# Kernel optimization log

Hardware: AMD Instinct MI355X
Metric: run time of the kernel (lower is better)

## Reference

```python
import jax, jax.numpy as jnp
import numpy as np

N_NODES = 50000
N_EDGES = 600000
IN_CH = 128
OUT_CH = 128


def setup_inputs() -> dict:
    key = jax.random.key(0)
    k1, k2, k3, k4 = jax.random.split(key, 4)
    x = jax.random.normal(k1, (N_NODES, IN_CH), dtype=jnp.float32)
    edge_index = jax.random.randint(k2, (2, N_EDGES), 0, N_NODES, dtype=jnp.int64)
    W_msg = jax.random.normal(k3, (OUT_CH, IN_CH * 9), dtype=jnp.float32) * (1.0 / np.sqrt(IN_CH * 9))
    b_msg = jnp.zeros((OUT_CH,), dtype=jnp.float32)
    W_root = jax.random.normal(k4, (OUT_CH, IN_CH), dtype=jnp.float32) * (1.0 / np.sqrt(IN_CH))
    b_root = jnp.zeros((OUT_CH,), dtype=jnp.float32)
    return {"x": x, "edge_index": edge_index, "W_msg": W_msg, "b_msg": b_msg,
            "W_root": W_root, "b_root": b_root}


def reference(x, edge_index, W_msg, b_msg, W_root, b_root):
    n = x.shape[0]
    src = edge_index[0]
    dst = edge_index[1]

    # in-degree per destination node
    degree = jax.ops.segment_sum(jnp.ones_like(dst, dtype=x.dtype), dst, num_segments=n)  # [N]

    msgs = x[src]  # [E, C] gathered source features
    agg_sum = jax.ops.segment_sum(msgs, dst, num_segments=n)                 # [N, C]
    agg_mean = agg_sum / jnp.maximum(degree, 1.0)[:, None]                    # [N, C]
    agg_max = jax.ops.segment_max(msgs, dst, num_segments=n)                  # [N, C], -inf for empty
    agg_max = jnp.where(degree[:, None] > 0, agg_max, 0.0)

    degree_term = jnp.log1p(degree + 1.0)[:, None]                            # [N, 1]
    degree_reference = jnp.maximum(jnp.mean(jnp.log1p(degree + 1.0)), 1.0)    # scalar

    amp = degree_term / degree_reference                                       # [N, 1]
    att = degree_reference / jnp.maximum(degree_term, 1e-06)                   # [N, 1]

    feats = []
    for agg in (agg_sum, agg_mean, agg_max):
        feats.append(agg)            # identity
        feats.append(agg * amp)      # amplification
        feats.append(agg * att)      # attenuation
    stacked = jnp.concatenate(feats, axis=-1)                                  # [N, 9C]

    return stacked @ W_msg.T + b_msg + x @ W_root.T + b_root
```

## Files before the change

### kernel.cpp

```cpp
#include <hip/hip_runtime.h>
#include <cmath>

#define IN_CH 128
#define OUT_CH 128
#define KDIM 512
#define NGEMM 384
#define GBM 256
#define GBN 192
#define SLOT_B 40960
#define SLOT_US 20480
#define PIPE_LDS_BYTES (3 * SLOT_B)

typedef __attribute__((ext_vector_type(8))) short bfrag;
typedef __attribute__((ext_vector_type(4))) float f32x4;

__device__ __forceinline__ unsigned short f2bf(float f) {
    unsigned int u = __float_as_uint(f);
    return (unsigned short)((u + 0x7FFFu + ((u >> 16) & 1u)) >> 16);
}
__device__ __forceinline__ float bf2f(unsigned short h) {
    return __uint_as_float(((unsigned int)h) << 16);
}
__device__ __forceinline__ float4 unpack4(uint2 u) {
    float4 r;
    r.x = __uint_as_float(u.x << 16);
    r.y = __uint_as_float(u.x & 0xFFFF0000u);
    r.z = __uint_as_float(u.y << 16);
    r.w = __uint_as_float(u.y & 0xFFFF0000u);
    return r;
}

__device__ __forceinline__ void gl2lds16(const void* g, void* l) {
    __builtin_amdgcn_global_load_lds(
        (const __attribute__((address_space(1))) unsigned int*)g,
        (__attribute__((address_space(3))) unsigned int*)l, 16, 0, 0);
}


__global__ void degree_kernel(const int* __restrict__ ei, int* __restrict__ degree, int E) {
    int e = blockIdx.x * blockDim.x + threadIdx.x;
    if (e < E) atomicAdd(&degree[ei[E + e]], 1);
}

__global__ __launch_bounds__(256) void scan1_kernel(const int* __restrict__ degree,
                                                    int* __restrict__ part,
                                                    float* __restrict__ partlog, int n) {
    int i = blockIdx.x * 256 + threadIdx.x;
    int d = (i < n) ? degree[i] : 0;
    float lg = (i < n) ? logf((float)d + 2.0f) : 0.f;
    #pragma unroll
    for (int off = 32; off; off >>= 1) {
        d += __shfl_down(d, off);
        lg += __shfl_down(lg, off);
    }
    __shared__ int sd[4];
    __shared__ float sl[4];
    int wv = threadIdx.x >> 6;
    if ((threadIdx.x & 63) == 0) { sd[wv] = d; sl[wv] = lg; }
    __syncthreads();
    if (threadIdx.x == 0) {
        part[blockIdx.x] = (sd[0] + sd[1]) + (sd[2] + sd[3]);
        partlog[blockIdx.x] = (sl[0] + sl[1]) + (sl[2] + sl[3]);
    }
}

__global__ __launch_bounds__(256) void scan2_kernel(int* __restrict__ part,
                                                    const float* __restrict__ partlog,
                                                    float* __restrict__ logsum, int B) {
    int tid = threadIdx.x, lane = tid & 63, wv = tid >> 6;
    __shared__ int wsum[4];
    __shared__ float wl[4];
    __shared__ int carry_s;
    if (tid == 0) carry_s = 0;
    float lg = 0.f;
    __syncthreads();
    for (int base0 = 0; base0 < B; base0 += 256) {
        int idx = base0 + tid;
        int v = (idx < B) ? part[idx] : 0;
        if (idx < B) lg += partlog[idx];
        int s = v;
        #pragma unroll
        for (int off = 1; off < 64; off <<= 1) {
            int t = __shfl_up(s, off);
            if (lane >= off) s += t;
        }
        if (lane == 63) wsum[wv] = s;
        __syncthreads();
        int wbase = carry_s;
        for (int w2 = 0; w2 < wv; ++w2) wbase += wsum[w2];
        if (idx < B) part[idx] = wbase + s - v;
        __syncthreads();
        if (tid == 0) carry_s += (wsum[0] + wsum[1]) + (wsum[2] + wsum[3]);
        __syncthreads();
    }
    #pragma unroll
    for (int off = 32; off; off >>= 1) lg += __shfl_down(lg, off);
    if (lane == 0) wl[wv] = lg;
    __syncthreads();
    if (tid == 0) logsum[0] = (wl[0] + wl[1]) + (wl[2] + wl[3]);
}

__global__ __launch_bounds__(256) void scan3_kernel(const int* __restrict__ degree,
                                                    const int* __restrict__ part,
                                                    int* __restrict__ offsets, int n, int E) {
    int i = blockIdx.x * 256 + threadIdx.x;
    int d = (i < n) ? degree[i] : 0;
    int lane = threadIdx.x & 63, wv = threadIdx.x >> 6;
    int s = d;
    #pragma unroll
    for (int off = 1; off < 64; off <<= 1) {
        int t = __shfl_up(s, off);
        if (lane >= off) s += t;
    }
    __shared__ int wsum[4];
    if (lane == 63) wsum[wv] = s;
    __syncthreads();
    int base = part[blockIdx.x];
    for (int w2 = 0; w2 < wv; ++w2) base += wsum[w2];
    if (i < n) offsets[i] = base + s - d;
    if (i == n - 1) offsets[n] = E;
}

__global__ void fill_kernel(const int* __restrict__ ei, int* __restrict__ offsets,
                            int* __restrict__ csr_src, int E) {
    int e = blockIdx.x * blockDim.x + threadIdx.x;
    if (e < E) {
        int src = ei[e];
        int dst = ei[E + e];
        int pos = atomicAdd(&offsets[dst], 1);
        csr_src[pos] = src;
    }
}


__global__ void xcast_kernel(const float* __restrict__ x, unsigned short* __restrict__ xb,
                             int total4) {
    int i = blockIdx.x * 256 + threadIdx.x;
    if (i >= total4) return;
    float4 v = ((const float4*)x)[i];
    uint2 p;
    p.x = (unsigned)f2bf(v.x) | ((unsigned)f2bf(v.y) << 16);
    p.y = (unsigned)f2bf(v.z) | ((unsigned)f2bf(v.w) << 16);
    ((uint2*)xb)[i] = p;
}


__global__ __launch_bounds__(256) void agg_kernel(const unsigned short* __restrict__ xb,
                                                  const int* __restrict__ csr_src,
                                                  const int* __restrict__ offsets,
                                                  const int* __restrict__ degree,
                                                  const float* __restrict__ logsum,
                                                  unsigned short* __restrict__ Zhi,
                                                  float* __restrict__ ampv,
                                                  float* __restrict__ attv,
                                                  int N, int Mpad) {
    int node = (blockIdx.x * 256 + threadIdx.x) >> 6;
    int lane = threadIdx.x & 63;
    if (node >= Mpad) return;
    int h = lane >> 5;
    int c4 = lane & 31;
    long zbase = (long)node * KDIM + c4 * 4;
    if (node >= N) {
        if (h == 0) {
            uint2 z = make_uint2(0u, 0u);
            #pragma unroll
            for (int sec = 0; sec < 4; ++sec) *(uint2*)&Zhi[zbase + sec * 128] = z;
        }
        return;
    }
    int deg = degree[node];
    int end = offsets[node];
    int beg = end - deg;
    const float NEG = -3.402823466e38f;
    float4 s[4], m[4];
    #pragma unroll
    for (int u = 0; u < 4; ++u) {
        s[u] = make_float4(0.f, 0.f, 0.f, 0.f);
        m[u] = make_float4(NEG, NEG, NEG, NEG);
    }
    int i = beg;
    for (; i + 8 <= end; i += 8) {
        int idx[4];
        #pragma unroll
        for (int u = 0; u < 4; ++u) idx[u] = csr_src[i + u * 2 + h];
        uint2 raw[4];
        #pragma unroll
        for (int u = 0; u < 4; ++u) raw[u] = *(const uint2*)&xb[(long)idx[u] * IN_CH + c4 * 4];
        #pragma unroll
        for (int u = 0; u < 4; ++u) {
            float4 v = unpack4(raw[u]);
            s[u].x += v.x; s[u].y += v.y; s[u].z += v.z; s[u].w += v.w;
            m[u].x = fmaxf(m[u].x, v.x); m[u].y = fmaxf(m[u].y, v.y);
            m[u].z = fmaxf(m[u].z, v.z); m[u].w = fmaxf(m[u].w, v.w);
        }
    }
    for (; i < end; i += 2) {
        int e = i + h;
        if (e < end) {
            float4 v = unpack4(*(const uint2*)&xb[(long)csr_src[e] * IN_CH + c4 * 4]);
            s[0].x += v.x; s[0].y += v.y; s[0].z += v.z; s[0].w += v.w;
            m[0].x = fmaxf(m[0].x, v.x); m[0].y = fmaxf(m[0].y, v.y);
            m[0].z = fmaxf(m[0].z, v.z); m[0].w = fmaxf(m[0].w, v.w);
        }
    }
    float4 sum, mx;
    sum.x = (s[0].x + s[1].x) + (s[2].x + s[3].x);
    sum.y = (s[0].y + s[1].y) + (s[2].y + s[3].y);
    sum.z = (s[0].z + s[1].z) + (s[2].z + s[3].z);
    sum.w = (s[0].w + s[1].w) + (s[2].w + s[3].w);
    mx.x = fmaxf(fmaxf(m[0].x, m[1].x), fmaxf(m[2].x, m[3].x));
    mx.y = fmaxf(fmaxf(m[0].y, m[1].y), fmaxf(m[2].y, m[3].y));
    mx.z = fmaxf(fmaxf(m[0].z, m[1].z), fmaxf(m[2].z, m[3].z));
    mx.w = fmaxf(fmaxf(m[0].w, m[1].w), fmaxf(m[2].w, m[3].w));
    sum.x += __shfl_xor(sum.x, 32); sum.y += __shfl_xor(sum.y, 32);
    sum.z += __shfl_xor(sum.z, 32); sum.w += __shfl_xor(sum.w, 32);
    mx.x = fmaxf(mx.x, __shfl_xor(mx.x, 32)); mx.y = fmaxf(mx.y, __shfl_xor(mx.y, 32));
    mx.z = fmaxf(mx.z, __shfl_xor(mx.z, 32)); mx.w = fmaxf(mx.w, __shfl_xor(mx.w, 32));

    float inv = 1.0f / fmaxf((float)deg, 1.0f);
    float4 mean = make_float4(sum.x * inv, sum.y * inv, sum.z * inv, sum.w * inv);
    if (deg == 0) mx = make_float4(0.f, 0.f, 0.f, 0.f);
    float4 xv = unpack4(*(const uint2*)&xb[(long)node * IN_CH + c4 * 4]);

    if (h == 0) {
        float4 secs[4] = { xv, sum, mean, mx };
        #pragma unroll
        for (int sec = 0; sec < 4; ++sec) {
            float4 v = secs[sec];
            uint2 hi;
            hi.x = (unsigned)f2bf(v.x) | ((unsigned)f2bf(v.y) << 16);
            hi.y = (unsigned)f2bf(v.z) | ((unsigned)f2bf(v.w) << 16);
            *(uint2*)&Zhi[zbase + sec * 128] = hi;
        }
    }
    if (lane == 0) {
        float ref = fmaxf(logsum[0] / (float)N, 1.0f);
        float dt = log1pf((float)deg + 1.0f);
        ampv[node] = dt / ref;
        attv[node] = ref / fmaxf(dt, 1e-6f);
    }
}


__global__ void wbuild_kernel(const float* __restrict__ Wmsg, const float* __restrict__ Wroot,
                              unsigned short* __restrict__ Whi, unsigned short* __restrict__ Wlo) {
    int idx = blockIdx.x * 256 + threadIdx.x;
    if (idx >= NGEMM * KDIM) return;
    int jp = idx >> 9;
    int k = idx & 511;
    int cg = jp / 96;
    int rem = jp - cg * 96;
    int s16 = rem >> 4;
    int r16 = rem & 15;
    int wn2 = s16 / 3;
    int sec = s16 - wn2 * 3;
    int ocol = cg * 32 + wn2 * 16 + r16;
    float v;
    if (k < 128) {
        v = (sec == 0) ? Wroot[ocol * 128 + k] : 0.f;
    } else {
        int a = (k - 128) >> 7;
        int c = (k - 128) & 127;
        v = Wmsg[ocol * 1152 + (a * 3 + sec) * 128 + c];
    }
    unsigned short h = f2bf(v);
    Whi[idx] = h;
    Wlo[idx] = f2bf(v - bf2f(h));
}


__global__ __launch_bounds__(1024, 4) void gemm_pipe(const unsigned short* __restrict__ Zhi,
                                                     const unsigned short* __restrict__ Whi,
                                                     const unsigned short* __restrict__ Wlo,
                                                     const float* __restrict__ ampv,
                                                     const float* __restrict__ attv,
                                                     const float* __restrict__ bmsg,
                                                     const float* __restrict__ broot,
                                                     float* __restrict__ out, int M) {
    extern __shared__ char smem[];
    unsigned short* lds = (unsigned short*)smem;
    const int tid = threadIdx.x;
    const int w = tid >> 6;
    const int lane = tid & 63;
    const int r16 = lane & 15, q = lane >> 4;
    const int wm = w >> 2, wn = w & 3;
    const int row0 = blockIdx.x * GBM;
    const int cg2 = blockIdx.y;

    const unsigned short* sAh = Zhi + (long)(row0 + w * 16 + r16) * KDIM + q * 8;
    const unsigned short* sB2 = (w < 12)
        ? Whi + (long)(cg2 * GBN + w * 16 + r16) * KDIM + q * 8
        : Wlo + (long)(cg2 * GBN + (w - 12) * 16 + r16) * KDIM + q * 8;
    const unsigned short* sB3 = Wlo + (long)(cg2 * GBN + (4 + w) * 16 + r16) * KDIM + q * 8;
    const int d0 = tid * 16, d2 = (1024 + tid) * 16, d3 = (2048 + tid) * 16;

    gl2lds16(sAh, smem + d0); gl2lds16(sB2, smem + d2); if (w < 8) gl2lds16(sB3, smem + d3);
    sAh += 32; sB2 += 32; sB3 += 32;
    gl2lds16(sAh, smem + SLOT_B + d0); gl2lds16(sB2, smem + SLOT_B + d2);
    if (w < 8) gl2lds16(sB3, smem + SLOT_B + d3);
    sAh += 32; sB2 += 32; sB3 += 32;

    if (w < 8) __builtin_amdgcn_s_waitcnt(0x0F73);
    else       __builtin_amdgcn_s_waitcnt(0x0F72);
    __builtin_amdgcn_s_barrier();
    __builtin_amdgcn_sched_barrier(0);

    f32x4 acc[4][3] = {};
    const int jtb = (wn >> 1) * 6 + (wn & 1) * 3;

    #pragma unroll 1
    for (int it = 0; it < 16; ++it) {
        const int s = it % 3;
        if (it + 2 < 16) {
            char* b = smem + ((it + 2) % 3) * SLOT_B;
            gl2lds16(sAh, b + d0); gl2lds16(sB2, b + d2); if (w < 8) gl2lds16(sB3, b + d3);
            sAh += 32; sB2 += 32; sB3 += 32;
        }
        const unsigned short* L = lds + s * SLOT_US;

        bfrag bh[3], bl[3];
        #pragma unroll
        for (int nt = 0; nt < 3; ++nt) {
            int chb = (jtb + nt) * 512 + lane * 8;
            bh[nt] = *(const bfrag*)&L[8192 + chb];
            bl[nt] = *(const bfrag*)&L[14336 + chb];
        }
        #pragma unroll
        for (int mt = 0; mt < 4; ++mt) {
            bfrag ah = *(const bfrag*)&L[((wm * 4 + mt) * 64 + lane) * 8];
            #pragma unroll
            for (int nt = 0; nt < 3; ++nt) {
                acc[mt][nt] = __builtin_amdgcn_mfma_f32_16x16x32_bf16(ah, bh[nt], acc[mt][nt], 0, 0, 0);
                acc[mt][nt] = __builtin_amdgcn_mfma_f32_16x16x32_bf16(ah, bl[nt], acc[mt][nt], 0, 0, 0);
            }
        }

        if (it < 14) {
            if (w < 8) __builtin_amdgcn_s_waitcnt(0x0F73);
            else       __builtin_amdgcn_s_waitcnt(0x0F72);
        } else if (it == 14) {
            __builtin_amdgcn_s_waitcnt(0x0F70);
        }
        if (it < 15) {
            __builtin_amdgcn_s_barrier();
            __builtin_amdgcn_sched_barrier(0);
        }
    }

    const int col = (cg2 * 2 + (wn >> 1)) * 32 + (wn & 1) * 16 + r16;
    const float bias = bmsg[col] + broot[col];
    #pragma unroll
    for (int mt = 0; mt < 4; ++mt) {
        #pragma unroll
        for (int r = 0; r < 4; ++r) {
            int row = row0 + wm * 64 + mt * 16 + q * 4 + r;
            if (row < M) {
                float v = acc[mt][0][r]
                        + ampv[row] * acc[mt][1][r]
                        + attv[row] * acc[mt][2][r] + bias;
                out[(long)row * OUT_CH + col] = v;
            }
        }
    }
}


__global__ __launch_bounds__(1024, 4) void gemm_sb(const unsigned short* __restrict__ Zhi,
                                                   const unsigned short* __restrict__ Whi,
                                                   const unsigned short* __restrict__ Wlo,
                                                   const float* __restrict__ ampv,
                                                   const float* __restrict__ attv,
                                                   const float* __restrict__ bmsg,
                                                   const float* __restrict__ broot,
                                                   float* __restrict__ out, int M) {
    __shared__ unsigned short lds[SLOT_US];
    const int tid = threadIdx.x;
    const int w = tid >> 6;
    const int lane = tid & 63;
    const int r16 = lane & 15, q = lane >> 4;
    const int wm = w >> 2, wn = w & 3;
    const int row0 = blockIdx.x * GBM;
    const int cg2 = blockIdx.y;

    const unsigned short* sAh = Zhi + (long)(row0 + w * 16 + r16) * KDIM + q * 8;
    const unsigned short* sB2 = (w < 12)
        ? Whi + (long)(cg2 * GBN + w * 16 + r16) * KDIM + q * 8
        : Wlo + (long)(cg2 * GBN + (w - 12) * 16 + r16) * KDIM + q * 8;
    const unsigned short* sB3 = Wlo + (long)(cg2 * GBN + (4 + w) * 16 + r16) * KDIM + q * 8;
    char* ldsb = (char*)lds;
    const int d0 = tid * 16, d2 = (1024 + tid) * 16, d3 = (2048 + tid) * 16;

    f32x4 acc[4][3] = {};
    const int jtb = (wn >> 1) * 6 + (wn & 1) * 3;

    #pragma unroll 1
    for (int it = 0; it < 16; ++it) {
        if (it) __syncthreads();
        gl2lds16(sAh, ldsb + d0); gl2lds16(sB2, ldsb + d2); if (w < 8) gl2lds16(sB3, ldsb + d3);
        sAh += 32; sB2 += 32; sB3 += 32;
        __syncthreads();

        bfrag bh[3], bl[3];
        #pragma unroll
        for (int nt = 0; nt < 3; ++nt) {
            int chb = (jtb + nt) * 512 + lane * 8;
            bh[nt] = *(const bfrag*)&lds[8192 + chb];
            bl[nt] = *(const bfrag*)&lds[14336 + chb];
        }
        #pragma unroll
        for (int mt = 0; mt < 4; ++mt) {
            bfrag ah = *(const bfrag*)&lds[((wm * 4 + mt) * 64 + lane) * 8];
            #pragma unroll
            for (int nt = 0; nt < 3; ++nt) {
                acc[mt][nt] = __builtin_amdgcn_mfma_f32_16x16x32_bf16(ah, bh[nt], acc[mt][nt], 0, 0, 0);
                acc[mt][nt] = __builtin_amdgcn_mfma_f32_16x16x32_bf16(ah, bl[nt], acc[mt][nt], 0, 0, 0);
            }
        }
    }

    const int col = (cg2 * 2 + (wn >> 1)) * 32 + (wn & 1) * 16 + r16;
    const float bias = bmsg[col] + broot[col];
    #pragma unroll
    for (int mt = 0; mt < 4; ++mt) {
        #pragma unroll
        for (int r = 0; r < 4; ++r) {
            int row = row0 + wm * 64 + mt * 16 + q * 4 + r;
            if (row < M) {
                float v = acc[mt][0][r]
                        + ampv[row] * acc[mt][1][r]
                        + attv[row] * acc[mt][2][r] + bias;
                out[(long)row * OUT_CH + col] = v;
            }
        }
    }
}


extern "C" void kernel_launch(void* const* d_in, const int* in_sizes, int n_in,
                              void* d_out, int out_size, void* d_ws, size_t ws_size,
                              hipStream_t stream) {
    const float* x     = (const float*)d_in[0];
    const int*   ei    = (const int*)d_in[1];
    const float* Wmsg  = (const float*)d_in[2];
    const float* bmsg  = (const float*)d_in[3];
    const float* Wroot = (const float*)d_in[4];
    const float* broot = (const float*)d_in[5];
    float* out = (float*)d_out;

    int N = in_sizes[0] / IN_CH;
    int E = in_sizes[1] / 2;
    int Mb = (N + GBM - 1) / GBM;
    int Mpad = Mb * GBM;
    int Sb = (N + 255) / 256;

    char* ws = (char*)d_ws;
    size_t off = 0;
    auto alloc = [&](size_t bytes) -> void* {
        void* p = ws + off;
        off = (off + bytes + 255) & ~(size_t)255;
        return p;
    };
    int* degree  = (int*)alloc((size_t)N * 4);
    int* offsets = (int*)alloc((size_t)(N + 1) * 4);
    float* logsum = (float*)alloc(4);
    int* part    = (int*)alloc((size_t)Sb * 4);
    float* partlog = (float*)alloc((size_t)Sb * 4);
    int* csr_src = (int*)alloc((size_t)E * 4);
    unsigned short* Whi = (unsigned short*)alloc((size_t)NGEMM * KDIM * 2);
    unsigned short* Wlo = (unsigned short*)alloc((size_t)NGEMM * KDIM * 2);
    unsigned short* Zhi = (unsigned short*)alloc((size_t)Mpad * KDIM * 2);
    unsigned short* xb  = (unsigned short*)alloc((size_t)Mpad * IN_CH * 2);
    float* ampv = (float*)alloc((size_t)N * 4);
    float* attv = (float*)alloc((size_t)N * 4);

    hipMemsetAsync(degree, 0, (size_t)N * 4, stream);

    degree_kernel<<<(E + 255) / 256, 256, 0, stream>>>(ei, degree, E);
    xcast_kernel<<<(N * IN_CH / 4 + 255) / 256, 256, 0, stream>>>(x, xb, N * IN_CH / 4);
    scan1_kernel<<<Sb, 256, 0, stream>>>(degree, part, partlog, N);
    scan2_kernel<<<1, 256, 0, stream>>>(part, partlog, logsum, Sb);
    scan3_kernel<<<Sb, 256, 0, stream>>>(degree, part, offsets, N, E);
    fill_kernel<<<(E + 255) / 256, 256, 0, stream>>>(ei, offsets, csr_src, E);
    agg_kernel<<<(Mpad * 64 + 255) / 256, 256, 0, stream>>>(xb, csr_src, offsets, degree, logsum,
                                                            Zhi, ampv, attv, N, Mpad);
    wbuild_kernel<<<(NGEMM * KDIM + 255) / 256, 256, 0, stream>>>(Wmsg, Wroot, Whi, Wlo);

    bool pipe = false;
    int dev = 0;
    if (hipGetDevice(&dev) == hipSuccess) {
        int optin = 0;
        if (hipDeviceGetAttribute(&optin, hipDeviceAttributeSharedMemPerBlockOptin, dev) == hipSuccess
            && optin >= (int)PIPE_LDS_BYTES) {
            pipe = (hipFuncSetAttribute((const void*)gemm_pipe,
                                        hipFuncAttributeMaxDynamicSharedMemorySize,
                                        PIPE_LDS_BYTES) == hipSuccess);
        }
    }
    dim3 ggrid(Mb, 2);
    if (pipe) {
        gemm_pipe<<<ggrid, 1024, PIPE_LDS_BYTES, stream>>>(Zhi, Whi, Wlo, ampv, attv,
                                                           bmsg, broot, out, N);
    } else {
        gemm_sb<<<ggrid, 1024, 0, stream>>>(Zhi, Whi, Wlo, ampv, attv,
                                            bmsg, broot, out, N);
    }
}
```

Before: 247.5 us.

## Shrink GEMM tile to 128 rows with 512 threads and double buffering

Replaces the 1024-thread, 256-row, triple-buffered pipelined GEMM with a 512-thread, 128-row variant that uses two LDS slots and reassigns the B-tile load mapping so each wave loads three 16-row chunks. Halving the M tile doubles the block count, which is meant to improve CU occupancy and load balance across the device. The LDS footprint drops from 120KB to 64KB, so more blocks may fit per CU. In exchange, prefetch depth falls from two stages to one, so global-to-LDS latency is less hidden, and each B tile is reloaded by twice as many blocks.

```diff
diff --git a/kernel.cpp b/kernel.cpp
--- a/kernel.cpp
+++ b/kernel.cpp
@@ -6,10 +6,13 @@
 #define KDIM 512
 #define NGEMM 384
 #define GBM 256
+#define GBM2 128
 #define GBN 192
 #define SLOT_B 40960
 #define SLOT_US 20480
-#define PIPE_LDS_BYTES (3 * SLOT_B)
+#define SLOT2_B 32768
+#define SLOT2_US 16384
+#define PIPE2_LDS_BYTES (2 * SLOT2_B)
 
 typedef __attribute__((ext_vector_type(8))) short bfrag;
 typedef __attribute__((ext_vector_type(4))) float f32x4;
@@ -269,7 +272,7 @@
 }
 
 
-__global__ __launch_bounds__(1024, 4) void gemm_pipe(const unsigned short* __restrict__ Zhi,
+__global__ __launch_bounds__(512, 4) void gemm_pipe2(const unsigned short* __restrict__ Zhi,
                                                      const unsigned short* __restrict__ Whi,
                                                      const unsigned short* __restrict__ Wlo,
                                                      const float* __restrict__ ampv,
@@ -284,24 +287,34 @@
     const int lane = tid & 63;
     const int r16 = lane & 15, q = lane >> 4;
     const int wm = w >> 2, wn = w & 3;
-    const int row0 = blockIdx.x * GBM;
+    const int row0 = blockIdx.x * GBM2;
     const int cg2 = blockIdx.y;
 
-    const unsigned short* sAh = Zhi + (long)(row0 + w * 16 + r16) * KDIM + q * 8;
-    const unsigned short* sB2 = (w < 12)
-        ? Whi + (long)(cg2 * GBN + w * 16 + r16) * KDIM + q * 8
-        : Wlo + (long)(cg2 * GBN + (w - 12) * 16 + r16) * KDIM + q * 8;
-    const unsigned short* sB3 = Wlo + (long)(cg2 * GBN + (4 + w) * 16 + r16) * KDIM + q * 8;
-    const int d0 = tid * 16, d2 = (1024 + tid) * 16, d3 = (2048 + tid) * 16;
-
-    gl2lds16(sAh, smem + d0); gl2lds16(sB2, smem + d2); if (w < 8) gl2lds16(sB3, smem + d3);
-    sAh += 32; sB2 += 32; sB3 += 32;
-    gl2lds16(sAh, smem + SLOT_B + d0); gl2lds16(sB2, smem + SLOT_B + d2);
-    if (w < 8) gl2lds16(sB3, smem + SLOT_B + d3);
-    sAh += 32; sB2 += 32; sB3 += 32;
-
-    if (w < 8) __builtin_amdgcn_s_waitcnt(0x0F73);
-    else       __builtin_amdgcn_s_waitcnt(0x0F72);
+    const unsigned short* sA = Zhi + (long)(row0 + w * 16 + r16) * KDIM + q * 8;
+    const unsigned short* sB0;
+    const unsigned short* sB1;
+    const unsigned short* sB2;
+    {
+        int b0 = w * 3;
+        const unsigned short* p[3];
+        #pragma unroll
+        for (int j = 0; j < 3; ++j) {
+            int b = b0 + j;
+            const unsigned short* Wb = (b < 12) ? Whi : Wlo;
+            int rrow = ((b < 12) ? b : (b - 12)) * 16;
+            p[j] = Wb + (long)(cg2 * GBN + rrow + r16) * KDIM + q * 8;
+        }
+        sB0 = p[0]; sB1 = p[1]; sB2 = p[2];
+    }
+    const int dA = tid * 16;
+    const int dB0 = 8192 + (w * 3 + 0) * 1024 + lane * 16;
+    const int dB1 = 8192 + (w * 3 + 1) * 1024 + lane * 16;
+    const int dB2 = 8192 + (w * 3 + 2) * 1024 + lane * 16;
+
+    gl2lds16(sA, smem + dA); gl2lds16(sB0, smem + dB0);
+    gl2lds16(sB1, smem + dB1); gl2lds16(sB2, smem + dB2);
+    sA += 32; sB0 += 32; sB1 += 32; sB2 += 32;
+    __builtin_amdgcn_s_waitcnt(0x0F70);
     __builtin_amdgcn_s_barrier();
     __builtin_amdgcn_sched_barrier(0);
 
@@ -310,20 +323,21 @@
 
     #pragma unroll 1
     for (int it = 0; it < 16; ++it) {
-        const int s = it % 3;
-        if (it + 2 < 16) {
-            char* b = smem + ((it + 2) % 3) * SLOT_B;
-            gl2lds16(sAh, b + d0); gl2lds16(sB2, b + d2); if (w < 8) gl2lds16(sB3, b + d3);
-            sAh += 32; sB2 += 32; sB3 += 32;
-        }
-        const unsigned short* L = lds + s * SLOT_US;
+        const int s = it & 1;
+        if (it + 1 < 16) {
+            char* b = smem + (s ^ 1) * SLOT2_B;
+            gl2lds16(sA, b + dA); gl2lds16(sB0, b + dB0);
+            gl2lds16(sB1, b + dB1); gl2lds16(sB2, b + dB2);
+            sA += 32; sB0 += 32; sB1 += 32; sB2 += 32;
+        }
+        const unsigned short* L = lds + s * SLOT2_US;
 
         bfrag bh[3], bl[3];
         #pragma unroll
         for (int nt = 0; nt < 3; ++nt) {
             int chb = (jtb + nt) * 512 + lane * 8;
-            bh[nt] = *(const bfrag*)&L[8192 + chb];
-            bl[nt] = *(const bfrag*)&L[14336 + chb];
+            bh[nt] = *(const bfrag*)&L[4096 + chb];
+            bl[nt] = *(const bfrag*)&L[10240 + chb];
         }
         #pragma unroll
         for (int mt = 0; mt < 4; ++mt) {
@@ -335,12 +349,7 @@
             }
         }
 
-        if (it < 14) {
-            if (w < 8) __builtin_amdgcn_s_waitcnt(0x0F73);
-            else       __builtin_amdgcn_s_waitcnt(0x0F72);
-        } else if (it == 14) {
-            __builtin_amdgcn_s_waitcnt(0x0F70);
-        }
+        if (it + 1 < 16) __builtin_amdgcn_s_waitcnt(0x0F70);
         if (it < 15) {
             __builtin_amdgcn_s_barrier();
             __builtin_amdgcn_sched_barrier(0);
@@ -451,6 +460,7 @@
     int E = in_sizes[1] / 2;
     int Mb = (N + GBM - 1) / GBM;
     int Mpad = Mb * GBM;
+    int Mb2 = (N + GBM2 - 1) / GBM2;
     int Sb = (N + 255) / 256;
 
     char* ws = (char*)d_ws;
@@ -490,17 +500,18 @@
     if (hipGetDevice(&dev) == hipSuccess) {
         int optin = 0;
         if (hipDeviceGetAttribute(&optin, hipDeviceAttributeSharedMemPerBlockOptin, dev) == hipSuccess
-            && optin >= (int)PIPE_LDS_BYTES) {
-            pipe = (hipFuncSetAttribute((const void*)gemm_pipe,
+            && optin >= (int)PIPE2_LDS_BYTES) {
+            pipe = (hipFuncSetAttribute((const void*)gemm_pipe2,
                                         hipFuncAttributeMaxDynamicSharedMemorySize,
-                                        PIPE_LDS_BYTES) == hipSuccess);
-        }
-    }
-    dim3 ggrid(Mb, 2);
+                                        PIPE2_LDS_BYTES) == hipSuccess);
+        }
+    }
     if (pipe) {
-        gemm_pipe<<<ggrid, 1024, PIPE_LDS_BYTES, stream>>>(Zhi, Whi, Wlo, ampv, attv,
-                                                           bmsg, broot, out, N);
+        dim3 ggrid(Mb2, 2);
+        gemm_pipe2<<<ggrid, 512, PIPE2_LDS_BYTES, stream>>>(Zhi, Whi, Wlo, ampv, attv,
+                                                            bmsg, broot, out, N);
     } else {
+        dim3 ggrid(Mb, 2);
         gemm_sb<<<ggrid, 1024, 0, stream>>>(Zhi, Whi, Wlo, ampv, attv,
                                             bmsg, broot, out, N);
     }
```

New measurement: 267.9 us. 1.08x slower.

## Rewrite pipelined GEMM with 32x32x16 MFMA and 512-thread blocks

Applied to the files above, without the earlier changes.

Replaces the 1024-thread pipelined GEMM, which used 16x16x32 bf16 MFMAs, with a 512-thread variant built on 32x32x16 MFMAs. Each wave now computes a 64x32 output tile with larger accumulators. The LDS fragment layout and the global-to-LDS copy assignment are redone so that hi and lo weight fragments sit p*6144 apart. The goal is fewer LDS fragment reads per MFMA and higher MFMA efficiency, at the cost of more accumulator registers per wave and fewer waves per block.

```diff
diff --git a/kernel.cpp b/kernel.cpp
--- a/kernel.cpp
+++ b/kernel.cpp
@@ -13,6 +13,7 @@
 
 typedef __attribute__((ext_vector_type(8))) short bfrag;
 typedef __attribute__((ext_vector_type(4))) float f32x4;
+typedef __attribute__((ext_vector_type(16))) float f32x16;
 
 __device__ __forceinline__ unsigned short f2bf(float f) {
     unsigned int u = __float_as_uint(f);
@@ -269,95 +270,104 @@
 }
 
 
-__global__ __launch_bounds__(1024, 4) void gemm_pipe(const unsigned short* __restrict__ Zhi,
-                                                     const unsigned short* __restrict__ Whi,
-                                                     const unsigned short* __restrict__ Wlo,
-                                                     const float* __restrict__ ampv,
-                                                     const float* __restrict__ attv,
-                                                     const float* __restrict__ bmsg,
-                                                     const float* __restrict__ broot,
-                                                     float* __restrict__ out, int M) {
+__global__ __launch_bounds__(512, 2) void gemm_pipe32(const unsigned short* __restrict__ Zhi,
+                                                      const unsigned short* __restrict__ Whi,
+                                                      const unsigned short* __restrict__ Wlo,
+                                                      const float* __restrict__ ampv,
+                                                      const float* __restrict__ attv,
+                                                      const float* __restrict__ bmsg,
+                                                      const float* __restrict__ broot,
+                                                      float* __restrict__ out, int M) {
     extern __shared__ char smem[];
     unsigned short* lds = (unsigned short*)smem;
     const int tid = threadIdx.x;
     const int w = tid >> 6;
     const int lane = tid & 63;
-    const int r16 = lane & 15, q = lane >> 4;
-    const int wm = w >> 2, wn = w & 3;
+    const int r16s = lane & 15, qs = lane >> 4;
+    const int wm = w >> 1, wn = w & 1;
     const int row0 = blockIdx.x * GBM;
     const int cg2 = blockIdx.y;
 
-    const unsigned short* sAh = Zhi + (long)(row0 + w * 16 + r16) * KDIM + q * 8;
-    const unsigned short* sB2 = (w < 12)
-        ? Whi + (long)(cg2 * GBN + w * 16 + r16) * KDIM + q * 8
-        : Wlo + (long)(cg2 * GBN + (w - 12) * 16 + r16) * KDIM + q * 8;
-    const unsigned short* sB3 = Wlo + (long)(cg2 * GBN + (4 + w) * 16 + r16) * KDIM + q * 8;
-    const int d0 = tid * 16, d2 = (1024 + tid) * 16, d3 = (2048 + tid) * 16;
-
-    gl2lds16(sAh, smem + d0); gl2lds16(sB2, smem + d2); if (w < 8) gl2lds16(sB3, smem + d3);
-    sAh += 32; sB2 += 32; sB3 += 32;
-    gl2lds16(sAh, smem + SLOT_B + d0); gl2lds16(sB2, smem + SLOT_B + d2);
-    if (w < 8) gl2lds16(sB3, smem + SLOT_B + d3);
-    sAh += 32; sB2 += 32; sB3 += 32;
-
-    if (w < 8) __builtin_amdgcn_s_waitcnt(0x0F73);
-    else       __builtin_amdgcn_s_waitcnt(0x0F72);
+    const unsigned short* sA0 = Zhi + (long)(row0 + (2 * w) * 16 + r16s) * KDIM + qs * 8;
+    const unsigned short* sA1 = sA0 + 16 * KDIM;
+    const unsigned short* Bb = (w < 4) ? Whi : Wlo;
+    const int c0 = (w < 4) ? 3 * w : 3 * (w - 4);
+    const unsigned short* sB0 = Bb + (long)(cg2 * GBN + c0 * 16 + r16s) * KDIM + qs * 8;
+    const unsigned short* sB1 = sB0 + 16 * KDIM;
+    const unsigned short* sB2 = sB0 + 32 * KDIM;
+    const int dA0 = (2 * w) * 1024 + lane * 16, dA1 = dA0 + 1024;
+    const int dB0 = 16384 + (3 * w) * 1024 + lane * 16;
+    const int dB1 = dB0 + 1024, dB2 = dB0 + 2048;
+
+    gl2lds16(sA0, smem + dA0); gl2lds16(sA1, smem + dA1);
+    gl2lds16(sB0, smem + dB0); gl2lds16(sB1, smem + dB1); gl2lds16(sB2, smem + dB2);
+    sA0 += 32; sA1 += 32; sB0 += 32; sB1 += 32; sB2 += 32;
+    gl2lds16(sA0, smem + SLOT_B + dA0); gl2lds16(sA1, smem + SLOT_B + dA1);
+    gl2lds16(sB0, smem + SLOT_B + dB0); gl2lds16(sB1, smem + SLOT_B + dB1);
+    gl2lds16(sB2, smem + SLOT_B + dB2);
+    sA0 += 32; sA1 += 32; sB0 += 32; sB1 += 32; sB2 += 32;
+
+    __builtin_amdgcn_s_waitcnt(0x0F75);
     __builtin_amdgcn_s_barrier();
     __builtin_amdgcn_sched_barrier(0);
 
-    f32x4 acc[4][3] = {};
-    const int jtb = (wn >> 1) * 6 + (wn & 1) * 3;
+    const int wn2r = (lane >> 4) & 1, khr = lane >> 5, r16r = lane & 15;
+    const int aBase = wm * 2048 + wn2r * 512 + khr * 128 + r16r * 8;
+    const int bBase = 8192 + wn * 3072 + wn2r * 1536 + khr * 128 + r16r * 8;
+
+    f32x16 acc[2][3] = {};
 
     #pragma unroll 1
     for (int it = 0; it < 16; ++it) {
         const int s = it % 3;
         if (it + 2 < 16) {
             char* b = smem + ((it + 2) % 3) * SLOT_B;
-            gl2lds16(sAh, b + d0); gl2lds16(sB2, b + d2); if (w < 8) gl2lds16(sB3, b + d3);
-            sAh += 32; sB2 += 32; sB3 += 32;
+            gl2lds16(sA0, b + dA0); gl2lds16(sA1, b + dA1);
+            gl2lds16(sB0, b + dB0); gl2lds16(sB1, b + dB1); gl2lds16(sB2, b + dB2);
+            sA0 += 32; sA1 += 32; sB0 += 32; sB1 += 32; sB2 += 32;
         }
         const unsigned short* L = lds + s * SLOT_US;
 
-        bfrag bh[3], bl[3];
-        #pragma unroll
-        for (int nt = 0; nt < 3; ++nt) {
-            int chb = (jtb + nt) * 512 + lane * 8;
-            bh[nt] = *(const bfrag*)&L[8192 + chb];
-            bl[nt] = *(const bfrag*)&L[14336 + chb];
-        }
-        #pragma unroll
-        for (int mt = 0; mt < 4; ++mt) {
-            bfrag ah = *(const bfrag*)&L[((wm * 4 + mt) * 64 + lane) * 8];
+        bfrag a[2][2];
+        #pragma unroll
+        for (int mt = 0; mt < 2; ++mt)
             #pragma unroll
-            for (int nt = 0; nt < 3; ++nt) {
-                acc[mt][nt] = __builtin_amdgcn_mfma_f32_16x16x32_bf16(ah, bh[nt], acc[mt][nt], 0, 0, 0);
-                acc[mt][nt] = __builtin_amdgcn_mfma_f32_16x16x32_bf16(ah, bl[nt], acc[mt][nt], 0, 0, 0);
+            for (int kh = 0; kh < 2; ++kh)
+                a[mt][kh] = *(const bfrag*)&L[aBase + mt * 1024 + kh * 256];
+
+        #pragma unroll
+        for (int kh = 0; kh < 2; ++kh) {
+            #pragma unroll
+            for (int p = 0; p < 2; ++p) {
+                #pragma unroll
+                for (int sec = 0; sec < 3; ++sec) {
+                    bfrag bf = *(const bfrag*)&L[bBase + sec * 512 + kh * 256 + p * 6144];
+                    acc[0][sec] = __builtin_amdgcn_mfma_f32_32x32x16_bf16(a[0][kh], bf, acc[0][sec], 0, 0, 0);
+                    acc[1][sec] = __builtin_amdgcn_mfma_f32_32x32x16_bf16(a[1][kh], bf, acc[1][sec], 0, 0, 0);
+                }
             }
         }
 
-        if (it < 14) {
-            if (w < 8) __builtin_amdgcn_s_waitcnt(0x0F73);
-            else       __builtin_amdgcn_s_waitcnt(0x0F72);
-        } else if (it == 14) {
-            __builtin_amdgcn_s_waitcnt(0x0F70);
-        }
+        if (it < 14)      __builtin_amdgcn_s_waitcnt(0x0F75);
+        else if (it == 14) __builtin_amdgcn_s_waitcnt(0x0F70);
         if (it < 15) {
             __builtin_amdgcn_s_barrier();
             __builtin_amdgcn_sched_barrier(0);
         }
     }
 
-    const int col = (cg2 * 2 + (wn >> 1)) * 32 + (wn & 1) * 16 + r16;
+    const int col = (cg2 * 2 + wn) * 32 + (lane & 31);
     const float bias = bmsg[col] + broot[col];
+    const int rb = row0 + wm * 64 + 4 * (lane >> 5);
     #pragma unroll
-    for (int mt = 0; mt < 4; ++mt) {
-        #pragma unroll
-        for (int r = 0; r < 4; ++r) {
-            int row = row0 + wm * 64 + mt * 16 + q * 4 + r;
+    for (int mt = 0; mt < 2; ++mt) {
+        #pragma unroll
+        for (int reg = 0; reg < 16; ++reg) {
+            int row = rb + mt * 32 + (reg & 3) + 8 * (reg >> 2);
             if (row < M) {
-                float v = acc[mt][0][r]
-                        + ampv[row] * acc[mt][1][r]
-                        + attv[row] * acc[mt][2][r] + bias;
+                float v = acc[mt][0][reg]
+                        + ampv[row] * acc[mt][1][reg]
+                        + attv[row] * acc[mt][2][reg] + bias;
                 out[(long)row * OUT_CH + col] = v;
             }
         }
@@ -491,15 +501,15 @@
         int optin = 0;
         if (hipDeviceGetAttribute(&optin, hipDeviceAttributeSharedMemPerBlockOptin, dev) == hipSuccess
             && optin >= (int)PIPE_LDS_BYTES) {
-            pipe = (hipFuncSetAttribute((const void*)gemm_pipe,
+            pipe = (hipFuncSetAttribute((const void*)gemm_pipe32,
                                         hipFuncAttributeMaxDynamicSharedMemorySize,
                                         PIPE_LDS_BYTES) == hipSuccess);
         }
     }
     dim3 ggrid(Mb, 2);
     if (pipe) {
-        gemm_pipe<<<ggrid, 1024, PIPE_LDS_BYTES, stream>>>(Zhi, Whi, Wlo, ampv, attv,
-                                                           bmsg, broot, out, N);
+        gemm_pipe32<<<ggrid, 512, PIPE_LDS_BYTES, stream>>>(Zhi, Whi, Wlo, ampv, attv,
+                                                            bmsg, broot, out, N);
     } else {
         gemm_sb<<<ggrid, 1024, 0, stream>>>(Zhi, Whi, Wlo, ampv, attv,
                                             bmsg, broot, out, N);
```

New measurement: 258.1 us. 4.3% more time.

## Fuse prep kernels, drop serial scan pass, and trim early GEMM k-steps

Applied to the files above, without the earlier changes.

Merges the degree count and the x-to-bf16 cast into one prep kernel. Removes the single-block scan2 kernel: each scan3 block now sums the preceding block partials itself, and the log-degree total is accumulated with a float atomic in scan1. The GEMM main loop is split so the first four k-steps issue MFMAs for only one N sub-tile, apparently relying on zero blocks in the packed weight layout to skip work. This cuts launches and the serial scan, but the float atomic makes logsum order nondeterministic, and the GEMM skip is only correct if those weight blocks really are zero.

```diff
diff --git a/kernel.cpp b/kernel.cpp
--- a/kernel.cpp
+++ b/kernel.cpp
@@ -37,14 +37,27 @@
 }
 
 
-__global__ void degree_kernel(const int* __restrict__ ei, int* __restrict__ degree, int E) {
-    int e = blockIdx.x * blockDim.x + threadIdx.x;
-    if (e < E) atomicAdd(&degree[ei[E + e]], 1);
+__global__ __launch_bounds__(256) void prep_kernel(const int* __restrict__ ei,
+                                                   int* __restrict__ degree,
+                                                   float* __restrict__ logsum,
+                                                   const float* __restrict__ x,
+                                                   unsigned short* __restrict__ xb,
+                                                   int E, int total4) {
+    int i = blockIdx.x * 256 + threadIdx.x;
+    if (i == 0) logsum[0] = 0.f;
+    if (i < E) atomicAdd(&degree[ei[E + i]], 1);
+    if (i < total4) {
+        float4 v = ((const float4*)x)[i];
+        uint2 p;
+        p.x = (unsigned)f2bf(v.x) | ((unsigned)f2bf(v.y) << 16);
+        p.y = (unsigned)f2bf(v.z) | ((unsigned)f2bf(v.w) << 16);
+        ((uint2*)xb)[i] = p;
+    }
 }
 
 __global__ __launch_bounds__(256) void scan1_kernel(const int* __restrict__ degree,
                                                     int* __restrict__ part,
-                                                    float* __restrict__ partlog, int n) {
+                                                    float* __restrict__ logsum, int n) {
     int i = blockIdx.x * 256 + threadIdx.x;
     int d = (i < n) ? degree[i] : 0;
     float lg = (i < n) ? logf((float)d + 2.0f) : 0.f;
@@ -60,52 +73,28 @@
     __syncthreads();
     if (threadIdx.x == 0) {
         part[blockIdx.x] = (sd[0] + sd[1]) + (sd[2] + sd[3]);
-        partlog[blockIdx.x] = (sl[0] + sl[1]) + (sl[2] + sl[3]);
-    }
-}
-
-__global__ __launch_bounds__(256) void scan2_kernel(int* __restrict__ part,
-                                                    const float* __restrict__ partlog,
-                                                    float* __restrict__ logsum, int B) {
-    int tid = threadIdx.x, lane = tid & 63, wv = tid >> 6;
-    __shared__ int wsum[4];
-    __shared__ float wl[4];
-    __shared__ int carry_s;
-    if (tid == 0) carry_s = 0;
-    float lg = 0.f;
-    __syncthreads();
-    for (int base0 = 0; base0 < B; base0 += 256) {
-        int idx = base0 + tid;
-        int v = (idx < B) ? part[idx] : 0;
-        if (idx < B) lg += partlog[idx];
-        int s = v;
-        #pragma unroll
-        for (int off = 1; off < 64; off <<= 1) {
-            int t = __shfl_up(s, off);
-            if (lane >= off) s += t;
-        }
-        if (lane == 63) wsum[wv] = s;
-        __syncthreads();
-        int wbase = carry_s;
-        for (int w2 = 0; w2 < wv; ++w2) wbase += wsum[w2];
-        if (idx < B) part[idx] = wbase + s - v;
-        __syncthreads();
-        if (tid == 0) carry_s += (wsum[0] + wsum[1]) + (wsum[2] + wsum[3]);
-        __syncthreads();
-    }
-    #pragma unroll
-    for (int off = 32; off; off >>= 1) lg += __shfl_down(lg, off);
-    if (lane == 0) wl[wv] = lg;
-    __syncthreads();
-    if (tid == 0) logsum[0] = (wl[0] + wl[1]) + (wl[2] + wl[3]);
+        atomicAdd(&logsum[0], (sl[0] + sl[1]) + (sl[2] + sl[3]));
+    }
 }
 
 __global__ __launch_bounds__(256) void scan3_kernel(const int* __restrict__ degree,
                                                     const int* __restrict__ part,
-                                                    int* __restrict__ offsets, int n, int E) {
-    int i = blockIdx.x * 256 + threadIdx.x;
+                                                    int* __restrict__ offsets,
+                                                    int n, int E, int Sb) {
+    int tid = threadIdx.x;
+    int i = blockIdx.x * 256 + tid;
+    int b = blockIdx.x;
+    int acc0 = 0;
+    for (int j = tid; j < b; j += 256) acc0 += part[j];
+    #pragma unroll
+    for (int off = 32; off; off >>= 1) acc0 += __shfl_down(acc0, off);
+    __shared__ int bsum[4];
+    int lane = tid & 63, wv = tid >> 6;
+    if (lane == 0) bsum[wv] = acc0;
+    __syncthreads();
+    int base = (bsum[0] + bsum[1]) + (bsum[2] + bsum[3]);
+
     int d = (i < n) ? degree[i] : 0;
-    int lane = threadIdx.x & 63, wv = threadIdx.x >> 6;
     int s = d;
     #pragma unroll
     for (int off = 1; off < 64; off <<= 1) {
@@ -115,7 +104,6 @@
     __shared__ int wsum[4];
     if (lane == 63) wsum[wv] = s;
     __syncthreads();
-    int base = part[blockIdx.x];
     for (int w2 = 0; w2 < wv; ++w2) base += wsum[w2];
     if (i < n) offsets[i] = base + s - d;
     if (i == n - 1) offsets[n] = E;
@@ -130,18 +118,6 @@
         int pos = atomicAdd(&offsets[dst], 1);
         csr_src[pos] = src;
     }
-}
-
-
-__global__ void xcast_kernel(const float* __restrict__ x, unsigned short* __restrict__ xb,
-                             int total4) {
-    int i = blockIdx.x * 256 + threadIdx.x;
-    if (i >= total4) return;
-    float4 v = ((const float4*)x)[i];
-    uint2 p;
-    p.x = (unsigned)f2bf(v.x) | ((unsigned)f2bf(v.y) << 16);
-    p.y = (unsigned)f2bf(v.z) | ((unsigned)f2bf(v.w) << 16);
-    ((uint2*)xb)[i] = p;
 }
 
 
@@ -309,7 +285,33 @@
     const int jtb = (wn >> 1) * 6 + (wn & 1) * 3;
 
     #pragma unroll 1
-    for (int it = 0; it < 16; ++it) {
+    for (int it = 0; it < 4; ++it) {
+        const int s = it % 3;
+        {
+            char* b = smem + ((it + 2) % 3) * SLOT_B;
+            gl2lds16(sAh, b + d0); gl2lds16(sB2, b + d2); if (w < 8) gl2lds16(sB3, b + d3);
+            sAh += 32; sB2 += 32; sB3 += 32;
+        }
+        const unsigned short* L = lds + s * SLOT_US;
+
+        int chb = jtb * 512 + lane * 8;
+        bfrag bh0 = *(const bfrag*)&L[8192 + chb];
+        bfrag bl0 = *(const bfrag*)&L[14336 + chb];
+        #pragma unroll
+        for (int mt = 0; mt < 4; ++mt) {
+            bfrag ah = *(const bfrag*)&L[((wm * 4 + mt) * 64 + lane) * 8];
+            acc[mt][0] = __builtin_amdgcn_mfma_f32_16x16x32_bf16(ah, bh0, acc[mt][0], 0, 0, 0);
+            acc[mt][0] = __builtin_amdgcn_mfma_f32_16x16x32_bf16(ah, bl0, acc[mt][0], 0, 0, 0);
+        }
+
+        if (w < 8) __builtin_amdgcn_s_waitcnt(0x0F73);
+        else       __builtin_amdgcn_s_waitcnt(0x0F72);
+        __builtin_amdgcn_s_barrier();
+        __builtin_amdgcn_sched_barrier(0);
+    }
+
+    #pragma unroll 1
+    for (int it = 4; it < 16; ++it) {
         const int s = it % 3;
         if (it + 2 < 16) {
             char* b = smem + ((it + 2) % 3) * SLOT_B;
@@ -452,6 +454,7 @@
     int Mb = (N + GBM - 1) / GBM;
     int Mpad = Mb * GBM;
     int Sb = (N + 255) / 256;
+    int total4 = N * IN_CH / 4;
 
     char* ws = (char*)d_ws;
     size_t off = 0;
@@ -464,7 +467,6 @@
     int* offsets = (int*)alloc((size_t)(N + 1) * 4);
     float* logsum = (float*)alloc(4);
     int* part    = (int*)alloc((size_t)Sb * 4);
-    float* partlog = (float*)alloc((size_t)Sb * 4);
     int* csr_src = (int*)alloc((size_t)E * 4);
     unsigned short* Whi = (unsigned short*)alloc((size_t)NGEMM * KDIM * 2);
     unsigned short* Wlo = (unsigned short*)alloc((size_t)NGEMM * KDIM * 2);
@@ -475,11 +477,10 @@
 
     hipMemsetAsync(degree, 0, (size_t)N * 4, stream);
 
-    degree_kernel<<<(E + 255) / 256, 256, 0, stream>>>(ei, degree, E);
-    xcast_kernel<<<(N * IN_CH / 4 + 255) / 256, 256, 0, stream>>>(x, xb, N * IN_CH / 4);
-    scan1_kernel<<<Sb, 256, 0, stream>>>(degree, part, partlog, N);
-    scan2_kernel<<<1, 256, 0, stream>>>(part, partlog, logsum, Sb);
-    scan3_kernel<<<Sb, 256, 0, stream>>>(degree, part, offsets, N, E);
+    int prepg = (max(E, total4) + 255) / 256;
+    prep_kernel<<<prepg, 256, 0, stream>>>(ei, degree, logsum, x, xb, E, total4);
+    scan1_kernel<<<Sb, 256, 0, stream>>>(degree, part, logsum, N);
+    scan3_kernel<<<Sb, 256, 0, stream>>>(degree, part, offsets, N, E, Sb);
     fill_kernel<<<(E + 255) / 256, 256, 0, stream>>>(ei, offsets, csr_src, E);
     agg_kernel<<<(Mpad * 64 + 255) / 256, 256, 0, stream>>>(xb, csr_src, offsets, degree, logsum,
                                                             Zhi, ampv, attv, N, Mpad);
```

After: 242.7 us. No clear change (-1.9%).
